# Performance work log

Measured on AMD Instinct MI355X. Metric: run time of the kernel, lower is better.

## Reference

```python
import jax, jax.numpy as jnp
import numpy as np

N, E, M, A, D = 100000, 3200000, 4096, 32, 16
G, V1, V2, O1 = 10, 20, 10, 20


def _lin(key, fin, fout, scale=0.1):
    kw, kb = jax.random.split(key)
    W = jax.random.normal(kw, (fin, fout), jnp.float32) * scale
    b = jax.random.normal(kb, (fout,), jnp.float32) * scale
    return W, b


def setup_inputs():
    key = jax.random.key(0)
    ks = jax.random.split(key, 32)
    inp = {}
    inp["x1"] = jax.random.normal(ks[0], (N, 15), jnp.float32)
    inp["x2"] = jax.random.normal(ks[1], (4,), jnp.float32)
    inp["edges"] = jax.random.randint(ks[2], (2, E), 0, N)
    inp["attack_src"] = jax.random.randint(ks[3], (M, A), 0, N)
    inp["attack_dst"] = jax.random.randint(ks[4], (M, A), 0, N)
    inp["attack_armies"] = jax.random.uniform(ks[5], (M, A), jnp.float32, 1.0, 20.0)
    inp["deploy_target"] = jax.random.randint(ks[6], (M, D), 0, N)
    inp["deploy_armies"] = jax.random.uniform(ks[7], (M, D), jnp.float32, 1.0, 10.0)
    inp["init_W"], inp["init_b"] = _lin(ks[8], 15, G)
    for i, fin in zip((1, 2, 3), (G + 15, 2 * G + 15, 3 * G + 15)):
        k1, k2, k3, k4 = jax.random.split(ks[8 + i], 4)
        inp[f"g{i}_Wl"] = jax.random.normal(k1, (fin, G), jnp.float32) * 0.1
        inp[f"g{i}_Wr"] = jax.random.normal(k2, (fin, G), jnp.float32) * 0.1
        inp[f"g{i}_att"] = jax.random.normal(k3, (G,), jnp.float32) * 0.1
        inp[f"g{i}_b"] = jax.random.normal(k4, (G,), jnp.float32) * 0.1
    inp["vt_W"], inp["vt_b"] = _lin(ks[12], 15 + G + 4, V1)
    inp["va_W"], inp["va_b"] = _lin(ks[13], V1, 1)
    inp["vv_W"], inp["vv_b"] = _lin(ks[14], V1, V2)
    inp["vl_W"], inp["vl_b"] = _lin(ks[15], V2, 1)
    inp["at_W"], inp["at_b"] = _lin(ks[16], 48, O1)
    inp["dt_W"], inp["dt_b"] = _lin(ks[17], 23, O1)
    inp["oa_W"], inp["oa_b"] = _lin(ks[18], O1, 1)
    inp["ov_W"], inp["ov_b"] = _lin(ks[19], O1, 1)
    return inp


def _gatv2(x, src, dst, Wl, Wr, att, bias, n):
    # GATv2 (PyG defaults: heads=1, negative_slope=0.2); dropout omitted (eval mode)
    xl = x @ Wl  # source-side transform  [N, G]
    xr = x @ Wr  # target-side transform  [N, G]
    e = jax.nn.leaky_relu(xl[src] + xr[dst], 0.2) @ att  # [Etot]
    emax = jax.ops.segment_max(e, dst, num_segments=n)
    ex = jnp.exp(e - emax[dst])
    denom = jax.ops.segment_sum(ex, dst, num_segments=n)
    alpha = ex / denom[dst]  # edge softmax per target node
    return jax.ops.segment_sum(alpha[:, None] * xl[src], dst, num_segments=n) + bias


def _forward(x1, x2, edges, attack_src, attack_dst, attack_armies,
             deploy_target, deploy_armies, p):
    n = x1.shape[0]
    loop = jnp.arange(n)
    src = jnp.concatenate([edges[0], loop])  # add_self_loops (PyG default)
    dst = jnp.concatenate([edges[1], loop])
    x_ = jax.nn.relu(x1 @ p["init_W"] + p["init_b"])  # Dropout = identity in eval
    xa = jax.nn.relu(_gatv2(jnp.concatenate([x_, x1], 1), src, dst,
                            p["g1_Wl"], p["g1_Wr"], p["g1_att"], p["g1_b"], n))
    xb = jax.nn.relu(_gatv2(jnp.concatenate([xa, x_, x1], 1), src, dst,
                            p["g2_Wl"], p["g2_Wr"], p["g2_att"], p["g2_b"], n))
    xc = jax.nn.relu(_gatv2(jnp.concatenate([xb, xa, x_, x1], 1), src, dst,
                            p["g3_Wl"], p["g3_Wr"], p["g3_att"], p["g3_b"], n))
    # per-move order features, batched over all moves at once: [M,A,*] / [M,D,*]
    x1d = x1[attack_dst]  # [M, A, 15]
    extra = 0.6 * attack_armies - 0.7 * (x1d[..., 3] + x1d[..., 4])
    att_feat = jnp.concatenate([xc[attack_src], xc[attack_dst],
                                x1[attack_src][..., 3:], x1d[..., 1:],
                                attack_armies[..., None], extra[..., None]], -1)  # [M,A,48]
    dep_feat = jnp.concatenate([xc[deploy_target], x1[deploy_target][..., 3:],
                                deploy_armies[..., None]], -1)  # [M,D,23]
    orders = jax.nn.relu(jnp.concatenate(
        [att_feat @ p["at_W"] + p["at_b"], dep_feat @ p["dt_W"] + p["dt_b"]], 1))  # [M,A+D,O1]
    oattn = jax.nn.softmax(orders @ p["oa_W"] + p["oa_b"], axis=1)  # softmax over orders
    pm = jnp.sum(oattn * (orders @ p["ov_W"] + p["ov_b"]), axis=(1, 2))  # [M]
    # value head: attention-pool over nodes
    vfeat = jnp.concatenate([xc, x1, jnp.tile(x2, (n, 1))], 1)  # [N, 29]
    v = jax.nn.relu(vfeat @ p["vt_W"] + p["vt_b"])
    vattn = jax.nn.softmax(v @ p["va_W"] + p["va_b"], axis=0)
    vagg = jax.nn.relu(jnp.sum(vattn * (v @ p["vv_W"] + p["vv_b"]), axis=0))
    V = jnp.tanh(vagg @ p["vl_W"] + p["vl_b"]).reshape(())
    return V, jax.nn.log_softmax(pm)


def reference(x1, x2, edges, attack_src, attack_dst, attack_armies,
              deploy_target, deploy_armies,
              init_W, init_b,
              g1_Wl, g1_Wr, g1_att, g1_b,
              g2_Wl, g2_Wr, g2_att, g2_b,
              g3_Wl, g3_Wr, g3_att, g3_b,
              vt_W, vt_b, va_W, va_b, vv_W, vv_b, vl_W, vl_b,
              at_W, at_b, dt_W, dt_b, oa_W, oa_b, ov_W, ov_b):
    p = dict(init_W=init_W, init_b=init_b,
             g1_Wl=g1_Wl, g1_Wr=g1_Wr, g1_att=g1_att, g1_b=g1_b,
             g2_Wl=g2_Wl, g2_Wr=g2_Wr, g2_att=g2_att, g2_b=g2_b,
             g3_Wl=g3_Wl, g3_Wr=g3_Wr, g3_att=g3_att, g3_b=g3_b,
             vt_W=vt_W, vt_b=vt_b, va_W=va_W, va_b=va_b, vv_W=vv_W, vv_b=vv_b,
             vl_W=vl_W, vl_b=vl_b, at_W=at_W, at_b=at_b, dt_W=dt_W, dt_b=dt_b,
             oa_W=oa_W, oa_b=oa_b, ov_W=ov_W, ov_b=ov_b)
    return _forward(x1, x2, edges, attack_src, attack_dst, attack_armies,
                    deploy_target, deploy_armies, p)
```

## Files before the change

kernel.cpp:

```cpp
#include <hip/hip_runtime.h>
#include <math.h>


#define PAD 12
#define LP 8
#define MAXB 784

__device__ __forceinline__ float lrelu02(float v) { return v > 0.f ? v : 0.2f * v; }

__device__ __forceinline__ unsigned pk_bf16(float a, float b)
{
    unsigned ua = __float_as_uint(a), ub = __float_as_uint(b);
    ua += 0x7fffu + ((ua >> 16) & 1u);
    ub += 0x7fffu + ((ub >> 16) & 1u);
    return (ua >> 16) | (ub & 0xffff0000u);
}
__device__ __forceinline__ float bf_lo(unsigned u) { return __uint_as_float(u << 16); }
__device__ __forceinline__ float bf_hi(unsigned u) { return __uint_as_float(u & 0xffff0000u); }

__global__ void k_zero(int* __restrict__ gbucket, float* __restrict__ vsums, int NBK)
{
    int t = threadIdx.x;
    if (t < NBK) gbucket[t] = 0;
    if (t < 16) vsums[t] = 0.f;
}

template <int NS>
__device__ __forceinline__ void transform_body(
    int n, const float* __restrict__ s0, const float* __restrict__ s1,
    const float* __restrict__ s2, const float* __restrict__ x1,
    const float* __restrict__ Wl, const float* __restrict__ Wr,
    unsigned* __restrict__ XLb, float* __restrict__ XR)
{
    float al[10], ar[10];
#pragma unroll
    for (int g = 0; g < 10; ++g) { al[g] = 0.f; ar[g] = 0.f; }
    int o = 0;
#define TB_BLOCK(SP)                                                        \
    {                                                                       \
        const float4* pr = (const float4*)((SP) + n * PAD);                 \
        float4 v0 = pr[0], v1 = pr[1], v2 = pr[2];                          \
        float fv[10] = {v0.x, v0.y, v0.z, v0.w, v1.x, v1.y, v1.z, v1.w,     \
                        v2.x, v2.y};                                        \
        _Pragma("unroll") for (int k = 0; k < 10; ++k)                      \
        {                                                                   \
            _Pragma("unroll") for (int g = 0; g < 10; ++g)                  \
            {                                                               \
                al[g] += fv[k] * Wl[(o + k) * 10 + g];                      \
                ar[g] += fv[k] * Wr[(o + k) * 10 + g];                      \
            }                                                               \
        }                                                                   \
        o += 10;                                                            \
    }
    if constexpr (NS >= 1) TB_BLOCK(s0)
    if constexpr (NS >= 2) TB_BLOCK(s1)
    if constexpr (NS >= 3) TB_BLOCK(s2)
#undef TB_BLOCK
#pragma unroll
    for (int k = 0; k < 15; ++k) {
        float fv = x1[n * 15 + k];
#pragma unroll
        for (int g = 0; g < 10; ++g) {
            al[g] += fv * Wl[(o + k) * 10 + g];
            ar[g] += fv * Wr[(o + k) * 10 + g];
        }
    }
    uint4 q0;
    q0.x = pk_bf16(al[0], al[1]);
    q0.y = pk_bf16(al[2], al[3]);
    q0.z = pk_bf16(al[4], al[5]);
    q0.w = pk_bf16(al[6], al[7]);
    uint4 q1;
    q1.x = pk_bf16(al[8], al[9]);
    q1.y = 0; q1.z = 0; q1.w = 0;
    uint4* pb = (uint4*)(XLb + (size_t)n * LP);
    pb[0] = q0;
    pb[1] = q1;
    float4* po = (float4*)(XR + n * PAD);
    po[0] = make_float4(ar[0], ar[1], ar[2], ar[3]);
    po[1] = make_float4(ar[4], ar[5], ar[6], ar[7]);
    po[2] = make_float4(ar[8], ar[9], 0.f, 0.f);
}

__global__ __launch_bounds__(256) void k_a1_init(
    const int* __restrict__ edst, int E, int* __restrict__ gbucket,
    const float* __restrict__ x1, const float* __restrict__ W,
    const float* __restrict__ b, float* __restrict__ xo, int PA, int N, int NBK)
{
    if ((int)blockIdx.x < PA) {
        __shared__ int h[MAXB];
        for (int j = threadIdx.x; j < NBK; j += 256) h[j] = 0;
        __syncthreads();
        int base = blockIdx.x * 8192;
        for (int k = 0; k < 32; ++k) {
            int i = base + k * 256 + threadIdx.x;
            if (i < E) atomicAdd(&h[edst[i] >> 7], 1);
        }
        __syncthreads();
        for (int j = threadIdx.x; j < NBK; j += 256) {
            int c = h[j];
            if (c) atomicAdd(&gbucket[j], c);
        }
    } else {
        int n = ((int)blockIdx.x - PA) * 256 + (int)threadIdx.x;
        if (n >= N) return;
        float acc[10];
#pragma unroll
        for (int g = 0; g < 10; ++g) acc[g] = b[g];
#pragma unroll
        for (int k = 0; k < 15; ++k) {
            float fv = x1[n * 15 + k];
#pragma unroll
            for (int g = 0; g < 10; ++g) acc[g] += fv * W[k * 10 + g];
        }
        float4* po = (float4*)(xo + n * PAD);
        po[0] = make_float4(fmaxf(acc[0], 0.f), fmaxf(acc[1], 0.f),
                            fmaxf(acc[2], 0.f), fmaxf(acc[3], 0.f));
        po[1] = make_float4(fmaxf(acc[4], 0.f), fmaxf(acc[5], 0.f),
                            fmaxf(acc[6], 0.f), fmaxf(acc[7], 0.f));
        po[2] = make_float4(fmaxf(acc[8], 0.f), fmaxf(acc[9], 0.f), 0.f, 0.f);
    }
}

__global__ __launch_bounds__(1024) void k_bscan(
    const int* __restrict__ gbucket, int* __restrict__ pbase,
    int* __restrict__ sbase, int* __restrict__ gcur,
    int* __restrict__ rowptr, int N, int NBK)
{
    __shared__ int w1[16], w2[16];
    int t = threadIdx.x, lane = t & 63, wv = t >> 6;
    int cE = 0, cT = 0;
    if (t < NBK) {
        cE = gbucket[t];
        int nin = N - (t << 7);
        nin = nin < 0 ? 0 : (nin > 128 ? 128 : nin);
        cT = cE + nin;
    }
    int i1 = cE, i2 = cT;
#pragma unroll
    for (int off = 1; off < 64; off <<= 1) {
        int u1 = __shfl_up(i1, off), u2 = __shfl_up(i2, off);
        if (lane >= off) { i1 += u1; i2 += u2; }
    }
    if (lane == 63) { w1[wv] = i1; w2[wv] = i2; }
    __syncthreads();
    int o1 = 0, o2 = 0;
    for (int k = 0; k < wv; ++k) { o1 += w1[k]; o2 += w2[k]; }
    i1 += o1; i2 += o2;
    if (t < NBK) {
        int pb = i1 - cE, sb = i2 - cT;
        pbase[t] = pb;
        sbase[t] = sb;
        gcur[t] = pb;
        if (t == NBK - 1) { pbase[NBK] = i1; sbase[NBK] = i2; rowptr[N] = i2; }
    }
}

__global__ __launch_bounds__(256) void k_a2(
    const int* __restrict__ esrc, const int* __restrict__ edst, int E,
    int* __restrict__ gcur, unsigned* __restrict__ pairs, int NBK)
{
    __shared__ int h[MAXB];
    __shared__ int bs[MAXB];
    for (int j = threadIdx.x; j < NBK; j += 256) h[j] = 0;
    __syncthreads();
    int base = blockIdx.x * 8192;
    for (int k = 0; k < 32; ++k) {
        int i = base + k * 256 + threadIdx.x;
        if (i < E) atomicAdd(&h[edst[i] >> 7], 1);
    }
    __syncthreads();
    for (int j = threadIdx.x; j < NBK; j += 256) {
        int c = h[j];
        bs[j] = c ? atomicAdd(&gcur[j], c) : 0;
        h[j] = 0;
    }
    __syncthreads();
    for (int k = 0; k < 32; ++k) {
        int i = base + k * 256 + threadIdx.x;
        if (i < E) {
            int d = edst[i], s = esrc[i];
            int bkt = d >> 7;
            int off = atomicAdd(&h[bkt], 1);
            pairs[bs[bkt] + off] = (unsigned)s | ((unsigned)(d & 127) << 17);
        }
    }
}

__global__ __launch_bounds__(256) void k_b_tr1(
    const unsigned* __restrict__ pairs, const int* __restrict__ pbase,
    const int* __restrict__ sbase, int* __restrict__ rowptr,
    int* __restrict__ deg, int* __restrict__ sidx, int N, int NBK,
    const float* __restrict__ s0a, const float* __restrict__ x1,
    const float* __restrict__ Wl, const float* __restrict__ Wr,
    unsigned* __restrict__ XLb, float* __restrict__ XR, int NB)
{
    if ((int)blockIdx.x < NBK) {
        __shared__ int cnt[128];
        __shared__ int cur[128];
        __shared__ int wtot;
        int t = threadIdx.x;
        if (t < 128) cnt[t] = 0;
        __syncthreads();
        int b = blockIdx.x, p0 = pbase[b], p1 = pbase[b + 1], n0 = b << 7;
        int nn = N - n0; nn = nn < 0 ? 0 : (nn > 128 ? 128 : nn);
        for (int i = p0 + t; i < p1; i += 256) atomicAdd(&cnt[pairs[i] >> 17], 1);
        __syncthreads();
        int x = 0, incl = 0;
        if (t < 128) {
            x = cnt[t] + (t < nn ? 1 : 0);
            incl = x;
            int lane = t & 63;
#pragma unroll
            for (int off = 1; off < 64; off <<= 1) {
                int u = __shfl_up(incl, off);
                if (lane >= off) incl += u;
            }
            if (t == 63) wtot = incl;
        }
        __syncthreads();
        int sb = sbase[b];
        if (t < 128) {
            if (t >= 64) incl += wtot;
            int st = incl - x;
            if (t < nn) {
                int r = sb + st;
                rowptr[n0 + t] = r;
                deg[n0 + t] = cnt[t] + 1;
                sidx[r] = n0 + t;
                cur[t] = st + 1;
            } else {
                cur[t] = st;
            }
        }
        __syncthreads();
        for (int i = p0 + t; i < p1; i += 256) {
            unsigned w = pairs[i];
            int l = w >> 17, s = w & 0x1FFFF;
            int off = atomicAdd(&cur[l], 1);
            sidx[sb + off] = s;
        }
    } else {
        int n = ((int)blockIdx.x - NBK) * 256 + (int)threadIdx.x;
        if (n >= N) return;
        transform_body<1>(n, s0a, nullptr, nullptr, x1, Wl, Wr, XLb, XR);
    }
}

template <int NS>
__global__ __launch_bounds__(256) void k_transform(
    const float* __restrict__ s0, const float* __restrict__ s1,
    const float* __restrict__ s2, const float* __restrict__ x1,
    const float* __restrict__ Wl, const float* __restrict__ Wr,
    unsigned* __restrict__ XLb, float* __restrict__ XR, int N)
{
    int n = blockIdx.x * blockDim.x + threadIdx.x;
    if (n >= N) return;
    transform_body<NS>(n, s0, s1, s2, x1, Wl, Wr, XLb, XR);
}

__global__ __launch_bounds__(256) void k_gather(
    const int* __restrict__ rowptr, const int* __restrict__ deg,
    const int* __restrict__ sidx,
    const unsigned* __restrict__ XLb, const float* __restrict__ XR,
    const float* __restrict__ att, const float* __restrict__ b,
    float* __restrict__ xo, int N)
{
    int node = blockIdx.x * 16 + (threadIdx.x >> 4);
    int l16 = threadIdx.x & 15;
    float acc[10];
#pragma unroll
    for (int g = 0; g < 10; ++g) acc[g] = 0.f;
    float den = 0.f;
    float satt[10];
#pragma unroll
    for (int g = 0; g < 10; ++g) satt[g] = att[g];
    if (node < N) {
        const float4* pr = (const float4*)(XR + node * PAD);
        float4 r0 = pr[0], r1 = pr[1], r2 = pr[2];
        float xr[10] = {r0.x, r0.y, r0.z, r0.w, r1.x, r1.y, r1.z, r1.w, r2.x, r2.y};
        int start = rowptr[node];
        int dgr = deg[node];
        int j = l16;
        while (j + 16 < dgr) {
            int s0 = sidx[start + j];
            int s1 = sidx[start + j + 16];
            const unsigned* pl0 = XLb + (size_t)s0 * LP;
            const unsigned* pl1 = XLb + (size_t)s1 * LP;
            uint4 qa = *(const uint4*)pl0;
            unsigned qa4 = pl0[4];
            uint4 qb = *(const uint4*)pl1;
            unsigned qb4 = pl1[4];
            float xa[10] = {bf_lo(qa.x), bf_hi(qa.x), bf_lo(qa.y), bf_hi(qa.y),
                            bf_lo(qa.z), bf_hi(qa.z), bf_lo(qa.w), bf_hi(qa.w),
                            bf_lo(qa4), bf_hi(qa4)};
            float xb[10] = {bf_lo(qb.x), bf_hi(qb.x), bf_lo(qb.y), bf_hi(qb.y),
                            bf_lo(qb.z), bf_hi(qb.z), bf_lo(qb.w), bf_hi(qb.w),
                            bf_lo(qb4), bf_hi(qb4)};
            float ea = 0.f, eb = 0.f;
#pragma unroll
            for (int g = 0; g < 10; ++g) {
                ea += lrelu02(xa[g] + xr[g]) * satt[g];
                eb += lrelu02(xb[g] + xr[g]) * satt[g];
            }
            float exa = __expf(ea), exb = __expf(eb);
#pragma unroll
            for (int g = 0; g < 10; ++g) acc[g] += exa * xa[g] + exb * xb[g];
            den += exa + exb;
            j += 32;
        }
        if (j < dgr) {
            int s = sidx[start + j];
            const unsigned* pl = XLb + (size_t)s * LP;
            uint4 q = *(const uint4*)pl;
            unsigned q4 = pl[4];
            float xl[10] = {bf_lo(q.x), bf_hi(q.x), bf_lo(q.y), bf_hi(q.y),
                            bf_lo(q.z), bf_hi(q.z), bf_lo(q.w), bf_hi(q.w),
                            bf_lo(q4), bf_hi(q4)};
            float e = 0.f;
#pragma unroll
            for (int g = 0; g < 10; ++g) e += lrelu02(xl[g] + xr[g]) * satt[g];
            float ex = __expf(e);
#pragma unroll
            for (int g = 0; g < 10; ++g) acc[g] += ex * xl[g];
            den += ex;
        }
    }
#pragma unroll
    for (int off = 1; off < 16; off <<= 1) {
        den += __shfl_xor(den, off);
#pragma unroll
        for (int g = 0; g < 10; ++g) acc[g] += __shfl_xor(acc[g], off);
    }
    if (node < N && l16 == 0) {
        float inv = 1.f / den;
        float r[10];
#pragma unroll
        for (int g = 0; g < 10; ++g) r[g] = fmaxf(acc[g] * inv + b[g], 0.f);
        float4* po = (float4*)(xo + node * PAD);
        po[0] = make_float4(r[0], r[1], r[2], r[3]);
        po[1] = make_float4(r[4], r[5], r[6], r[7]);
        po[2] = make_float4(r[8], r[9], 0.f, 0.f);
    }
}

__global__ __launch_bounds__(256) void k_value_policy(
    const float* __restrict__ xc, const float* __restrict__ x1,
    const float* __restrict__ x2,
    const float* __restrict__ vtW, const float* __restrict__ vtb,
    const float* __restrict__ vaW, const float* __restrict__ vab,
    const float* __restrict__ vvW, const float* __restrict__ vvb,
    float* __restrict__ vsums,
    const int* __restrict__ asrc, const int* __restrict__ adst,
    const float* __restrict__ aarm,
    const int* __restrict__ dtgt, const float* __restrict__ darm,
    const float* __restrict__ atW, const float* __restrict__ atb,
    const float* __restrict__ dtW, const float* __restrict__ dtb,
    const float* __restrict__ oaW, const float* __restrict__ oab,
    const float* __restrict__ ovW, const float* __restrict__ ovb,
    float* __restrict__ pm, int NB, int N, int M)
{
    if ((int)blockIdx.x < NB) {
        __shared__ float sred[4][11];
        int t = threadIdx.x;
        int n = blockIdx.x * blockDim.x + t;
        float w = 0.f;
        float wv[10];
#pragma unroll
        for (int c = 0; c < 10; ++c) wv[c] = 0.f;
        if (n < N) {
            float v[20];
#pragma unroll
            for (int j = 0; j < 20; ++j) v[j] = vtb[j];
            {
                const float4* pc = (const float4*)(xc + n * PAD);
                float4 c0 = pc[0], c1 = pc[1], c2 = pc[2];
                float fv[10] = {c0.x, c0.y, c0.z, c0.w, c1.x, c1.y, c1.z, c1.w,
                                c2.x, c2.y};
#pragma unroll
                for (int k = 0; k < 10; ++k)
#pragma unroll
                    for (int j = 0; j < 20; ++j) v[j] += fv[k] * vtW[k * 20 + j];
            }
#pragma unroll
            for (int k = 0; k < 15; ++k) {
                float fv = x1[n * 15 + k];
#pragma unroll
                for (int j = 0; j < 20; ++j) v[j] += fv * vtW[(10 + k) * 20 + j];
            }
#pragma unroll
            for (int k = 0; k < 4; ++k) {
                float fv = x2[k];
#pragma unroll
                for (int j = 0; j < 20; ++j) v[j] += fv * vtW[(25 + k) * 20 + j];
            }
            float sc = vab[0];
#pragma unroll
            for (int j = 0; j < 20; ++j) {
                v[j] = fmaxf(v[j], 0.f);
                sc += v[j] * vaW[j];
            }
            w = __expf(sc);
#pragma unroll
            for (int c = 0; c < 10; ++c) {
                float t2 = vvb[c];
#pragma unroll
                for (int j = 0; j < 20; ++j) t2 += v[j] * vvW[j * 10 + c];
                wv[c] = w * t2;
            }
        }
#pragma unroll
        for (int off = 32; off > 0; off >>= 1) {
            w += __shfl_xor(w, off);
#pragma unroll
            for (int c = 0; c < 10; ++c) wv[c] += __shfl_xor(wv[c], off);
        }
        int wave = t >> 6, lane = t & 63;
        if (lane == 0) {
            sred[wave][0] = w;
#pragma unroll
            for (int c = 0; c < 10; ++c) sred[wave][1 + c] = wv[c];
        }
        __syncthreads();
        if (t == 0) {
#pragma unroll
            for (int c = 0; c < 11; ++c) {
                float s = sred[0][c] + sred[1][c] + sred[2][c] + sred[3][c];
                atomicAdd(&vsums[c], s);
            }
        }
    } else {
        int wave = threadIdx.x >> 6, lane = threadIdx.x & 63;
        int m = ((int)blockIdx.x - NB) * 4 + wave;
        float asc = -1e30f, vsc = 0.f;
        if (m < M) {
            float ord[20];
            bool have = false;
            if (lane < 32) {
                int a = lane;
                int s = asrc[m * 32 + a], d = adst[m * 32 + a];
                float arm = aarm[m * 32 + a];
#pragma unroll
                for (int j = 0; j < 20; ++j) ord[j] = atb[j];
                {
                    const float4* pc = (const float4*)(xc + s * PAD);
                    float4 c0 = pc[0], c1 = pc[1], c2 = pc[2];
                    float fv[10] = {c0.x, c0.y, c0.z, c0.w, c1.x, c1.y, c1.z,
                                    c1.w, c2.x, c2.y};
#pragma unroll
                    for (int k = 0; k < 10; ++k)
#pragma unroll
                        for (int j = 0; j < 20; ++j)
                            ord[j] += fv[k] * atW[k * 20 + j];
                }
                {
                    const float4* pc = (const float4*)(xc + d * PAD);
                    float4 c0 = pc[0], c1 = pc[1], c2 = pc[2];
                    float fv[10] = {c0.x, c0.y, c0.z, c0.w, c1.x, c1.y, c1.z,
                                    c1.w, c2.x, c2.y};
#pragma unroll
                    for (int k = 0; k < 10; ++k)
#pragma unroll
                        for (int j = 0; j < 20; ++j)
                            ord[j] += fv[k] * atW[(10 + k) * 20 + j];
                }
#pragma unroll
                for (int k = 0; k < 12; ++k) {
                    float fv = x1[s * 15 + 3 + k];
#pragma unroll
                    for (int j = 0; j < 20; ++j)
                        ord[j] += fv * atW[(20 + k) * 20 + j];
                }
                float d3 = 0.f, d4 = 0.f;
#pragma unroll
                for (int k = 0; k < 14; ++k) {
                    float fv = x1[d * 15 + 1 + k];
                    if (k == 2) d3 = fv;
                    if (k == 3) d4 = fv;
#pragma unroll
                    for (int j = 0; j < 20; ++j)
                        ord[j] += fv * atW[(32 + k) * 20 + j];
                }
                float extra = 0.6f * arm - 0.7f * (d3 + d4);
#pragma unroll
                for (int j = 0; j < 20; ++j)
                    ord[j] += arm * atW[46 * 20 + j] + extra * atW[47 * 20 + j];
                have = true;
            } else if (lane < 48) {
                int dd = lane - 32;
                int tg = dtgt[m * 16 + dd];
                float arm = darm[m * 16 + dd];
#pragma unroll
                for (int j = 0; j < 20; ++j) ord[j] = dtb[j];
                {
                    const float4* pc = (const float4*)(xc + tg * PAD);
                    float4 c0 = pc[0], c1 = pc[1], c2 = pc[2];
                    float fv[10] = {c0.x, c0.y, c0.z, c0.w, c1.x, c1.y, c1.z,
                                    c1.w, c2.x, c2.y};
#pragma unroll
                    for (int k = 0; k < 10; ++k)
#pragma unroll
                        for (int j = 0; j < 20; ++j)
                            ord[j] += fv[k] * dtW[k * 20 + j];
                }
#pragma unroll
                for (int k = 0; k < 12; ++k) {
                    float fv = x1[tg * 15 + 3 + k];
#pragma unroll
                    for (int j = 0; j < 20; ++j)
                        ord[j] += fv * dtW[(10 + k) * 20 + j];
                }
#pragma unroll
                for (int j = 0; j < 20; ++j) ord[j] += arm * dtW[22 * 20 + j];
                have = true;
            }
            if (have) {
                asc = oab[0]; vsc = ovb[0];
#pragma unroll
                for (int j = 0; j < 20; ++j) {
                    float oj = fmaxf(ord[j], 0.f);
                    asc += oj * oaW[j];
                    vsc += oj * ovW[j];
                }
            }
        }
        float mx = asc;
#pragma unroll
        for (int off = 32; off > 0; off >>= 1) mx = fmaxf(mx, __shfl_xor(mx, off));
        float p = (asc > -1e29f) ? __expf(asc - mx) : 0.f;
        float num = p * vsc;
        float Z = p;
#pragma unroll
        for (int off = 32; off > 0; off >>= 1) {
            Z += __shfl_xor(Z, off);
            num += __shfl_xor(num, off);
        }
        if (m < M && lane == 0) pm[m] = num / Z;
    }
}

__global__ __launch_bounds__(1024) void k_final(
    const float* __restrict__ pm, const float* __restrict__ vsums,
    const float* __restrict__ vlW, const float* __restrict__ vlb,
    float* __restrict__ out, int M)
{
    __shared__ float red[16];
    __shared__ float sval;
    int t = threadIdx.x;
    int wave = t >> 6, lane = t & 63;
    if (t == 1023) {
        float inv = 1.f / vsums[0];
        float V = vlb[0];
#pragma unroll
        for (int j = 0; j < 10; ++j) V += fmaxf(vsums[1 + j] * inv, 0.f) * vlW[j];
        out[0] = tanhf(V);
    }
    float mx = -1e30f;
    for (int i = t; i < M; i += 1024) mx = fmaxf(mx, pm[i]);
#pragma unroll
    for (int off = 32; off > 0; off >>= 1) mx = fmaxf(mx, __shfl_xor(mx, off));
    if (lane == 0) red[wave] = mx;
    __syncthreads();
    if (t == 0) {
        float m2 = red[0];
        for (int i = 1; i < 16; ++i) m2 = fmaxf(m2, red[i]);
        sval = m2;
    }
    __syncthreads();
    float smax = sval;
    float sum = 0.f;
    for (int i = t; i < M; i += 1024) sum += __expf(pm[i] - smax);
#pragma unroll
    for (int off = 32; off > 0; off >>= 1) sum += __shfl_xor(sum, off);
    if (lane == 0) red[wave] = sum;
    __syncthreads();
    if (t == 0) {
        float s2 = 0.f;
        for (int i = 0; i < 16; ++i) s2 += red[i];
        sval = s2;
    }
    __syncthreads();
    float lse = smax + logf(sval);
    for (int i = t; i < M; i += 1024) out[1 + i] = pm[i] - lse;
}

extern "C" void kernel_launch(void* const* d_in, const int* in_sizes, int n_in,
                              void* d_out, int out_size, void* d_ws, size_t ws_size,
                              hipStream_t stream)
{
    const float* x1   = (const float*)d_in[0];
    const float* x2   = (const float*)d_in[1];
    const int*   edges = (const int*)d_in[2];
    const int*   asrc = (const int*)d_in[3];
    const int*   adst = (const int*)d_in[4];
    const float* aarm = (const float*)d_in[5];
    const int*   dtgt = (const int*)d_in[6];
    const float* darm = (const float*)d_in[7];
    const float* initW = (const float*)d_in[8];
    const float* initb = (const float*)d_in[9];
    const float* g1Wl = (const float*)d_in[10];
    const float* g1Wr = (const float*)d_in[11];
    const float* g1att = (const float*)d_in[12];
    const float* g1b = (const float*)d_in[13];
    const float* g2Wl = (const float*)d_in[14];
    const float* g2Wr = (const float*)d_in[15];
    const float* g2att = (const float*)d_in[16];
    const float* g2b = (const float*)d_in[17];
    const float* g3Wl = (const float*)d_in[18];
    const float* g3Wr = (const float*)d_in[19];
    const float* g3att = (const float*)d_in[20];
    const float* g3b = (const float*)d_in[21];
    const float* vtW = (const float*)d_in[22];
    const float* vtb = (const float*)d_in[23];
    const float* vaW = (const float*)d_in[24];
    const float* vab = (const float*)d_in[25];
    const float* vvW = (const float*)d_in[26];
    const float* vvb = (const float*)d_in[27];
    const float* vlW = (const float*)d_in[28];
    const float* vlb = (const float*)d_in[29];
    const float* atW = (const float*)d_in[30];
    const float* atb = (const float*)d_in[31];
    const float* dtW = (const float*)d_in[32];
    const float* dtb = (const float*)d_in[33];
    const float* oaW = (const float*)d_in[34];
    const float* oab = (const float*)d_in[35];
    const float* ovW = (const float*)d_in[36];
    const float* ovb = (const float*)d_in[37];

    const int N = in_sizes[0] / 15;
    const int E = in_sizes[2] / 2;
    const int M = in_sizes[3] / 32;
    const int Etot = E + N;
    const int NBK = (N + 127) >> 7;

    float* ws = (float*)d_ws;
    size_t off = 0;
    float* XU = ws + off; off += (size_t)N * PAD;
    float* XA = ws + off; off += (size_t)N * PAD;
    float* XB = ws + off; off += (size_t)N * PAD;
    float* XC = ws + off; off += (size_t)N * PAD;
    unsigned* XLb = (unsigned*)(ws + off); off += (size_t)N * LP;
    float* XR = ws + off; off += (size_t)N * PAD;
    int* sidx = (int*)(ws + off); off += Etot;
    unsigned* pairs = (unsigned*)(ws + off); off += E;
    int* deg = (int*)(ws + off); off += N;
    int* rowptr = (int*)(ws + off); off += N + 8;
    int* gbucket = (int*)(ws + off); off += MAXB + 8;
    int* pbase = (int*)(ws + off); off += MAXB + 8;
    int* sbase = (int*)(ws + off); off += MAXB + 8;
    int* gcur = (int*)(ws + off); off += MAXB + 8;
    float* VS = ws + off; off += 16;
    float* PM = ws + off; off += M;

    float* outp = (float*)d_out;

    const int NB = (N + 255) / 256;
    const int PA = (E + 8191) / 8192;
    const int NG = (N + 15) / 16;
    const int PB = (M + 3) / 4;
    const int* esrc = edges;
    const int* edst = edges + E;

    k_zero<<<1, 1024, 0, stream>>>(gbucket, VS, NBK);
    k_a1_init<<<PA + NB, 256, 0, stream>>>(edst, E, gbucket, x1, initW, initb, XU, PA, N, NBK);
    k_bscan<<<1, 1024, 0, stream>>>(gbucket, pbase, sbase, gcur, rowptr, N, NBK);
    k_a2<<<PA, 256, 0, stream>>>(esrc, edst, E, gcur, pairs, NBK);
    k_b_tr1<<<NBK + NB, 256, 0, stream>>>(pairs, pbase, sbase, rowptr, deg, sidx, N, NBK,
                                          XU, x1, g1Wl, g1Wr, XLb, XR, NB);
    k_gather<<<NG, 256, 0, stream>>>(rowptr, deg, sidx, XLb, XR, g1att, g1b, XA, N);

    k_transform<2><<<NB, 256, 0, stream>>>(XA, XU, nullptr, x1, g2Wl, g2Wr, XLb, XR, N);
    k_gather<<<NG, 256, 0, stream>>>(rowptr, deg, sidx, XLb, XR, g2att, g2b, XB, N);

    k_transform<3><<<NB, 256, 0, stream>>>(XB, XA, XU, x1, g3Wl, g3Wr, XLb, XR, N);
    k_gather<<<NG, 256, 0, stream>>>(rowptr, deg, sidx, XLb, XR, g3att, g3b, XC, N);

    k_value_policy<<<NB + PB, 256, 0, stream>>>(XC, x1, x2, vtW, vtb, vaW, vab,
                                                vvW, vvb, VS, asrc, adst, aarm,
                                                dtgt, darm, atW, atb, dtW, dtb,
                                                oaW, oab, ovW, ovb, PM, NB, N, M);
    k_final<<<1, 1024, 0, stream>>>(PM, VS, vlW, vlb, outp, M);
}
```

Before: 409.1 us.

## Replace atomic bucket scatter with per-block count matrix scan and stable positions

The edge bucketing pass now records each edge's local rank within its block and bucket, and writes a full per-bucket, per-block count matrix instead of atomically accumulating global bucket counts. A three-kernel scan over that matrix produces exact, deterministic offsets. k_a2 then becomes a simple per-edge scatter that needs no histogram recompute and no global atomics. This removes the second read of edges and the atomic contention. In exchange it adds a 16-bit position array, aliased onto XA, plus the extra scan launches over a matrix of roughly 782×391 entries.

```diff
diff --git a/kernel.cpp b/kernel.cpp
--- a/kernel.cpp
+++ b/kernel.cpp
@@ -5,6 +5,7 @@
 #define PAD 12
 #define LP 8
 #define MAXB 784
+#define CHK 8192
 
 __device__ __forceinline__ float lrelu02(float v) { return v > 0.f ? v : 0.2f * v; }
 
@@ -17,13 +18,6 @@
 }
 __device__ __forceinline__ float bf_lo(unsigned u) { return __uint_as_float(u << 16); }
 __device__ __forceinline__ float bf_hi(unsigned u) { return __uint_as_float(u & 0xffff0000u); }
-
-__global__ void k_zero(int* __restrict__ gbucket, float* __restrict__ vsums, int NBK)
-{
-    int t = threadIdx.x;
-    if (t < NBK) gbucket[t] = 0;
-    if (t < 16) vsums[t] = 0.f;
-}
 
 template <int NS>
 __device__ __forceinline__ void transform_body(
@@ -83,24 +77,27 @@
 }
 
 __global__ __launch_bounds__(256) void k_a1_init(
-    const int* __restrict__ edst, int E, int* __restrict__ gbucket,
+    const int* __restrict__ edst, int E, unsigned short* __restrict__ pos,
+    int* __restrict__ cntg, int PA,
     const float* __restrict__ x1, const float* __restrict__ W,
-    const float* __restrict__ b, float* __restrict__ xo, int PA, int N, int NBK)
+    const float* __restrict__ b, float* __restrict__ xo, int N, int NBK)
 {
     if ((int)blockIdx.x < PA) {
         __shared__ int h[MAXB];
         for (int j = threadIdx.x; j < NBK; j += 256) h[j] = 0;
         __syncthreads();
-        int base = blockIdx.x * 8192;
-        for (int k = 0; k < 32; ++k) {
+        int base = blockIdx.x * CHK;
+        for (int k = 0; k < CHK / 256; ++k) {
             int i = base + k * 256 + threadIdx.x;
-            if (i < E) atomicAdd(&h[edst[i] >> 7], 1);
+            if (i < E) {
+                int bkt = edst[i] >> 7;
+                int p = atomicAdd(&h[bkt], 1);
+                pos[i] = (unsigned short)p;
+            }
         }
         __syncthreads();
-        for (int j = threadIdx.x; j < NBK; j += 256) {
-            int c = h[j];
-            if (c) atomicAdd(&gbucket[j], c);
-        }
+        for (int j = threadIdx.x; j < NBK; j += 256)
+            cntg[(size_t)j * PA + blockIdx.x] = h[j];
     } else {
         int n = ((int)blockIdx.x - PA) * 256 + (int)threadIdx.x;
         if (n >= N) return;
@@ -122,75 +119,79 @@
     }
 }
 
-__global__ __launch_bounds__(1024) void k_bscan(
-    const int* __restrict__ gbucket, int* __restrict__ pbase,
-    int* __restrict__ sbase, int* __restrict__ gcur,
-    int* __restrict__ rowptr, int N, int NBK)
-{
-    __shared__ int w1[16], w2[16];
-    int t = threadIdx.x, lane = t & 63, wv = t >> 6;
-    int cE = 0, cT = 0;
-    if (t < NBK) {
-        cE = gbucket[t];
-        int nin = N - (t << 7);
-        nin = nin < 0 ? 0 : (nin > 128 ? 128 : nin);
-        cT = cE + nin;
-    }
-    int i1 = cE, i2 = cT;
+__global__ __launch_bounds__(1024) void k_scanA(
+    const int* __restrict__ cntg, int* __restrict__ bases,
+    int* __restrict__ bsumA, int TOT)
+{
+    __shared__ int wsum[16];
+    int t = threadIdx.x;
+    int i = blockIdx.x * 1024 + t;
+    int lane = t & 63, w = t >> 6;
+    int x = (i < TOT) ? cntg[i] : 0;
+    int incl = x;
 #pragma unroll
     for (int off = 1; off < 64; off <<= 1) {
-        int u1 = __shfl_up(i1, off), u2 = __shfl_up(i2, off);
-        if (lane >= off) { i1 += u1; i2 += u2; }
-    }
-    if (lane == 63) { w1[wv] = i1; w2[wv] = i2; }
+        int u = __shfl_up(incl, off);
+        if (lane >= off) incl += u;
+    }
+    if (lane == 63) wsum[w] = incl;
     __syncthreads();
-    int o1 = 0, o2 = 0;
-    for (int k = 0; k < wv; ++k) { o1 += w1[k]; o2 += w2[k]; }
-    i1 += o1; i2 += o2;
-    if (t < NBK) {
-        int pb = i1 - cE, sb = i2 - cT;
-        pbase[t] = pb;
-        sbase[t] = sb;
-        gcur[t] = pb;
-        if (t == NBK - 1) { pbase[NBK] = i1; sbase[NBK] = i2; rowptr[N] = i2; }
-    }
+    int woff = 0;
+    for (int k = 0; k < w; ++k) woff += wsum[k];
+    incl += woff;
+    if (i < TOT) bases[i] = incl - x;
+    if (t == 1023) bsumA[blockIdx.x] = incl;
+}
+
+__global__ __launch_bounds__(512) void k_scanB(
+    const int* __restrict__ bsumA, int* __restrict__ boffA, int NBLKA,
+    float* __restrict__ vsums, int* __restrict__ rowptr, int N, int Etot)
+{
+    __shared__ int wsum[8];
+    int t = threadIdx.x;
+    int lane = t & 63, w = t >> 6;
+    int x = (t < NBLKA) ? bsumA[t] : 0;
+    int incl = x;
+#pragma unroll
+    for (int off = 1; off < 64; off <<= 1) {
+        int u = __shfl_up(incl, off);
+        if (lane >= off) incl += u;
+    }
+    if (lane == 63) wsum[w] = incl;
+    __syncthreads();
+    int woff = 0;
+    for (int k = 0; k < w; ++k) woff += wsum[k];
+    incl += woff;
+    if (t < NBLKA) boffA[t] = incl - x;
+    if (t < 16) vsums[t] = 0.f;
+    if (t == 0) rowptr[N] = Etot;
+}
+
+__global__ __launch_bounds__(1024) void k_scanC(
+    int* __restrict__ bases, const int* __restrict__ boffA, int TOT)
+{
+    int i = blockIdx.x * 1024 + threadIdx.x;
+    if (i < TOT) bases[i] += boffA[blockIdx.x];
 }
 
 __global__ __launch_bounds__(256) void k_a2(
     const int* __restrict__ esrc, const int* __restrict__ edst, int E,
-    int* __restrict__ gcur, unsigned* __restrict__ pairs, int NBK)
-{
-    __shared__ int h[MAXB];
-    __shared__ int bs[MAXB];
-    for (int j = threadIdx.x; j < NBK; j += 256) h[j] = 0;
-    __syncthreads();
-    int base = blockIdx.x * 8192;
-    for (int k = 0; k < 32; ++k) {
-        int i = base + k * 256 + threadIdx.x;
-        if (i < E) atomicAdd(&h[edst[i] >> 7], 1);
-    }
-    __syncthreads();
-    for (int j = threadIdx.x; j < NBK; j += 256) {
-        int c = h[j];
-        bs[j] = c ? atomicAdd(&gcur[j], c) : 0;
-        h[j] = 0;
-    }
-    __syncthreads();
-    for (int k = 0; k < 32; ++k) {
-        int i = base + k * 256 + threadIdx.x;
-        if (i < E) {
-            int d = edst[i], s = esrc[i];
-            int bkt = d >> 7;
-            int off = atomicAdd(&h[bkt], 1);
-            pairs[bs[bkt] + off] = (unsigned)s | ((unsigned)(d & 127) << 17);
-        }
-    }
+    const int* __restrict__ bases, const unsigned short* __restrict__ pos,
+    unsigned* __restrict__ pairs, int PA)
+{
+    int i = blockIdx.x * 256 + threadIdx.x;
+    if (i >= E) return;
+    int d = edst[i], s = esrc[i];
+    int bkt = d >> 7;
+    int blk = i / CHK;
+    int dest = bases[(size_t)bkt * PA + blk] + (int)pos[i];
+    pairs[dest] = (unsigned)s | ((unsigned)(d & 127) << 17);
 }
 
 __global__ __launch_bounds__(256) void k_b_tr1(
-    const unsigned* __restrict__ pairs, const int* __restrict__ pbase,
-    const int* __restrict__ sbase, int* __restrict__ rowptr,
-    int* __restrict__ deg, int* __restrict__ sidx, int N, int NBK,
+    const unsigned* __restrict__ pairs, const int* __restrict__ bases,
+    int* __restrict__ rowptr, int* __restrict__ deg, int* __restrict__ sidx,
+    int N, int NBK, int PA, int E,
     const float* __restrict__ s0a, const float* __restrict__ x1,
     const float* __restrict__ Wl, const float* __restrict__ Wr,
     unsigned* __restrict__ XLb, float* __restrict__ XR, int NB)
@@ -202,7 +203,10 @@
         int t = threadIdx.x;
         if (t < 128) cnt[t] = 0;
         __syncthreads();
-        int b = blockIdx.x, p0 = pbase[b], p1 = pbase[b + 1], n0 = b << 7;
+        int b = blockIdx.x;
+        int p0 = bases[(size_t)b * PA];
+        int p1 = (b + 1 < NBK) ? bases[(size_t)(b + 1) * PA] : E;
+        int n0 = b << 7;
         int nn = N - n0; nn = nn < 0 ? 0 : (nn > 128 ? 128 : nn);
         for (int i = p0 + t; i < p1; i += 256) atomicAdd(&cnt[pairs[i] >> 17], 1);
         __syncthreads();
@@ -219,7 +223,7 @@
             if (t == 63) wtot = incl;
         }
         __syncthreads();
-        int sb = sbase[b];
+        int sb = p0 + (b << 7);
         if (t < 128) {
             if (t >= 64) incl += wtot;
             int st = incl - x;
@@ -632,6 +636,8 @@
     const int M = in_sizes[3] / 32;
     const int Etot = E + N;
     const int NBK = (N + 127) >> 7;
+    const int PA = (E + CHK - 1) / CHK;
+    const int TOT = NBK * PA;
 
     float* ws = (float*)d_ws;
     size_t off = 0;
@@ -645,27 +651,30 @@
     unsigned* pairs = (unsigned*)(ws + off); off += E;
     int* deg = (int*)(ws + off); off += N;
     int* rowptr = (int*)(ws + off); off += N + 8;
-    int* gbucket = (int*)(ws + off); off += MAXB + 8;
-    int* pbase = (int*)(ws + off); off += MAXB + 8;
-    int* sbase = (int*)(ws + off); off += MAXB + 8;
-    int* gcur = (int*)(ws + off); off += MAXB + 8;
+    int* cntg = (int*)(ws + off); off += TOT + 8;
+    int* bases = (int*)(ws + off); off += TOT + 8;
+    int* bsumA = (int*)(ws + off); off += 512;
+    int* boffA = (int*)(ws + off); off += 512;
     float* VS = ws + off; off += 16;
     float* PM = ws + off; off += M;
+    unsigned short* pos = (unsigned short*)XA;
 
     float* outp = (float*)d_out;
 
     const int NB = (N + 255) / 256;
-    const int PA = (E + 8191) / 8192;
     const int NG = (N + 15) / 16;
     const int PB = (M + 3) / 4;
+    const int SCA = (TOT + 1023) / 1024;
     const int* esrc = edges;
     const int* edst = edges + E;
 
-    k_zero<<<1, 1024, 0, stream>>>(gbucket, VS, NBK);
-    k_a1_init<<<PA + NB, 256, 0, stream>>>(edst, E, gbucket, x1, initW, initb, XU, PA, N, NBK);
-    k_bscan<<<1, 1024, 0, stream>>>(gbucket, pbase, sbase, gcur, rowptr, N, NBK);
-    k_a2<<<PA, 256, 0, stream>>>(esrc, edst, E, gcur, pairs, NBK);
-    k_b_tr1<<<NBK + NB, 256, 0, stream>>>(pairs, pbase, sbase, rowptr, deg, sidx, N, NBK,
+    k_a1_init<<<PA + NB, 256, 0, stream>>>(edst, E, pos, cntg, PA,
+                                           x1, initW, initb, XU, N, NBK);
+    k_scanA<<<SCA, 1024, 0, stream>>>(cntg, bases, bsumA, TOT);
+    k_scanB<<<1, 512, 0, stream>>>(bsumA, boffA, SCA, VS, rowptr, N, Etot);
+    k_scanC<<<SCA, 1024, 0, stream>>>(bases, boffA, TOT);
+    k_a2<<<(E + 255) / 256, 256, 0, stream>>>(esrc, edst, E, bases, pos, pairs, PA);
+    k_b_tr1<<<NBK + NB, 256, 0, stream>>>(pairs, bases, rowptr, deg, sidx, N, NBK, PA, E,
                                           XU, x1, g1Wl, g1Wr, XLb, XR, NB);
     k_gather<<<NG, 256, 0, stream>>>(rowptr, deg, sidx, XLb, XR, g1att, g1b, XA, N);
 
```

Result: faster. 395.0 us (-3.4%).
